# Optimization experiments

Measured on AMD Instinct MI355X. Metric: run time of the kernel, lower is better.

Reference implementation:

```python
import jax, jax.numpy as jnp
import numpy as np

NEG_SLOPE = 0.01  # torch nn.LeakyReLU default


def setup_inputs() -> dict:
    key = jax.random.key(0)
    kq, kk, kv, km, kw = jax.random.split(key, 5)
    B, Lq, Lk, Dk, Dv = 4, 2048, 2048, 512, 512
    q = jax.random.normal(kq, (B, Lq, Dk), dtype=jnp.float32)
    k = jax.random.normal(kk, (B, Lk, Dk), dtype=jnp.float32)
    v = jax.random.normal(kv, (B, Lk, Dv), dtype=jnp.float32)
    attn_mask = jax.random.randint(km, (B, Lq, Lk), 0, 2).astype(jnp.int32)
    # xavier_normal for (Dk, 1): std = sqrt(2 / (Dk + 1))
    weight = jax.random.normal(kw, (Dk, 1), dtype=jnp.float32) * np.sqrt(2.0 / (Dk + 1))
    return {"q": q, "k": k, "v": v, "attn_mask": attn_mask, "weight": weight}


def reference(q, k, v, attn_mask, weight):
    # (q - k) @ w  ==  (q @ w) - (k @ w): avoid the [B,Lq,Lk,Dk] intermediate.
    qw = jnp.einsum('bqd,do->bq', q, weight)  # [B, Lq]
    kw = jnp.einsum('bkd,do->bk', k, weight)  # [B, Lk]
    scores = qw[:, :, None] - kw[:, None, :]  # [B, Lq, Lk]
    attn = jnp.where(scores >= 0, scores, NEG_SLOPE * scores)  # LeakyReLU
    masked = attn_mask == 0
    attn = jnp.where(masked, -jnp.inf, attn)
    attn = jax.nn.softmax(attn, axis=2)
    attn = jnp.where(masked, 0.0, attn)
    # dropout omitted (eval mode / identity for reference correctness)
    output = jnp.einsum('bqk,bkd->bqd', attn, v)  # bmm
    return output, attn
```

## Files before the change

### kernel.cpp

```cpp
#include <hip/hip_runtime.h>
#include <math.h>

#define BB 4
#define LQ 2048
#define LK 2048
#define DK 512
#define DV 512

typedef __attribute__((ext_vector_type(8))) _Float16 f16x8;
typedef __attribute__((ext_vector_type(2))) _Float16 f16x2;
typedef __attribute__((ext_vector_type(4))) float f32x4;

#define WS_QW    0
#define WS_KW    8192
#define WS_M     16384
#define WS_INV   24576
#define WS_VF16  32768
#define WS_PART  2129920
#define NOUT     ((size_t)BB * LQ * DV)
#define WS_NEED(nks) (((size_t)WS_PART + (size_t)(nks) * NOUT) * 4)

__device__ __forceinline__ unsigned int pk2(float a, float b) {
    auto h = __builtin_amdgcn_cvt_pkrtz(a, b);
    return __builtin_bit_cast(unsigned int, h);
}

__global__ __launch_bounds__(256) void qkw_kernel(const float* __restrict__ q,
                                                  const float* __restrict__ k,
                                                  const float* __restrict__ w,
                                                  float* __restrict__ ws) {
    int gw   = (int)((blockIdx.x * blockDim.x + threadIdx.x) >> 6);
    int lane = threadIdx.x & 63;
    const int nq = BB * LQ;
    const float* row = (gw < nq) ? (q + (size_t)gw * DK) : (k + (size_t)(gw - nq) * DK);

    float acc = 0.f;
#pragma unroll
    for (int j = 0; j < DK; j += 256) {
        int idx = j + lane * 4;
        float4 rv = *reinterpret_cast<const float4*>(row + idx);
        float4 wv = *reinterpret_cast<const float4*>(w + idx);
        acc += rv.x * wv.x + rv.y * wv.y + rv.z * wv.z + rv.w * wv.w;
    }
#pragma unroll
    for (int off = 32; off >= 1; off >>= 1) acc += __shfl_xor(acc, off, 64);
    if (lane == 0) ws[gw] = acc;
}

__global__ __launch_bounds__(256) void vpack_kernel(const float* __restrict__ v,
                                                    unsigned short* __restrict__ vF) {
    __shared__ float tile[32][517];
    const int k32 = blockIdx.x;
    const int b   = blockIdx.y;
    const int k0  = k32 * 32;
    const int t   = threadIdx.x;

#pragma unroll
    for (int i = 0; i < 16; ++i) {
        int flat = i * 256 + t;
        int row  = flat >> 7;
        int c4   = flat & 127;
        float4 f = *reinterpret_cast<const float4*>(
            v + ((size_t)(b * LK + k0 + row)) * DV + c4 * 4);
        tile[row][c4 * 4 + 0] = f.x;
        tile[row][c4 * 4 + 1] = f.y;
        tile[row][c4 * 4 + 2] = f.z;
        tile[row][c4 * 4 + 3] = f.w;
    }
    __syncthreads();

    const int w = t >> 6, l = t & 63;
    const int rbase = (l >> 4) * 8;
#pragma unroll
    for (int f = 0; f < 8; ++f) {
        int n16 = w * 8 + f;
        int col = n16 * 16 + (l & 15);
        f16x8 vv;
#pragma unroll
        for (int j = 0; j < 8; ++j) vv[j] = (_Float16)tile[rbase + j][col];
        size_t u16base = (((size_t)(b * 32 + n16)) * 64 + k32) * 512;
        *reinterpret_cast<f16x8*>(vF + u16base + l * 8) = vv;
    }
}

__global__ __launch_bounds__(256) void rowstat_kernel(const int* __restrict__ mask,
                                                      float* __restrict__ ws,
                                                      float* __restrict__ attn) {
    __shared__ float kws[LK];
    const int b = (blockIdx.x * 4) / LQ;
    const int t = threadIdx.x;

    const float4* kw4 = reinterpret_cast<const float4*>(ws + WS_KW + b * LK);
#pragma unroll
    for (int i = 0; i < 2; ++i)
        reinterpret_cast<float4*>(kws)[t + i * 256] = kw4[t + i * 256];
    __syncthreads();

    const int wave = t >> 6, lane = t & 63;
    const int rid  = blockIdx.x * 4 + wave;
    const float qwv = ws[WS_QW + rid];
    const int* mrow = mask + (size_t)rid * LK;

    float m = -INFINITY, s = 0.f;
    unsigned int mybits = 0;
#pragma unroll
    for (int i = 0; i < 8; ++i) {
        int e = (i * 64 + lane) * 4;
        int4  mi = *reinterpret_cast<const int4*>(mrow + e);
        float4 kv = reinterpret_cast<const float4*>(kws)[i * 64 + lane];
        float vals[4] = {kv.x, kv.y, kv.z, kv.w};
        int   msks[4] = {mi.x, mi.y, mi.z, mi.w};

        unsigned int bits = (msks[0] ? 1u : 0u) | (msks[1] ? 2u : 0u) |
                            (msks[2] ? 4u : 0u) | (msks[3] ? 8u : 0u);
        mybits |= bits << (i * 4);

#pragma unroll
        for (int j = 0; j < 4; ++j) {
            float sc = qwv - vals[j];
            sc = fmaxf(sc, 0.01f * sc);
            if (msks[j]) {
                if (sc > m) { s = s * __expf(m - sc) + 1.f; m = sc; }
                else        { s += __expf(sc - m); }
            }
        }
    }
#pragma unroll
    for (int off = 32; off >= 1; off >>= 1) {
        float mo = __shfl_xor(m, off, 64);
        float so = __shfl_xor(s, off, 64);
        float M  = fmaxf(m, mo);
        float sa = (m  == M) ? s  : s  * __expf(m  - M);
        float sb = (mo == M) ? so : so * __expf(mo - M);
        m = M; s = sa + sb;
    }
    const float inv = (s > 0.f) ? 1.f / s : 0.f;
    if (lane == 0) {
        ws[WS_M   + rid] = m;
        ws[WS_INV + rid] = inv;
    }

    float* arow = attn + (size_t)rid * LK;
#pragma unroll
    for (int i = 0; i < 8; ++i) {
        float4 kv = reinterpret_cast<const float4*>(kws)[i * 64 + lane];
        float vals[4] = {kv.x, kv.y, kv.z, kv.w};
        unsigned int bits = (mybits >> (i * 4)) & 0xFu;
        float p[4];
#pragma unroll
        for (int j = 0; j < 4; ++j) {
            float sc = qwv - vals[j];
            sc = fmaxf(sc, 0.01f * sc);
            p[j] = (bits & (1u << j)) ? __expf(sc - m) * inv : 0.f;
        }
        *reinterpret_cast<float4*>(arow + (i * 64 + lane) * 4) =
            make_float4(p[0], p[1], p[2], p[3]);
    }
}

__global__ __launch_bounds__(512, 2) void pv_kernel(
        const float* __restrict__ attn,
        const unsigned short* __restrict__ vF,
        float* __restrict__ dst,
        int nks) {
    __shared__ unsigned int pH32[2][1024];
    __shared__ unsigned int pL32[2][1024];

    const int bid = blockIdx.x;
    const int ks  = bid & (nks - 1);
    const int rst = bid / nks;
    const int b   = rst & 3;
    const int qt  = rst >> 2;
    const int kspan  = LK / nks;
    const int ksteps = kspan >> 5;
    const int kbase  = ks * kspan;
    float* dstk = dst + (size_t)ks * NOUT;

    const int t = threadIdx.x;
    const int w = t >> 6, l = t & 63;

    const int m0   = t >> 8;
    const int lp   = (t >> 2) & 63;
    const int jp   = t & 3;
    const int row0 = m0 * 16 + (lp & 15);
    const int kk   = ((lp >> 4) << 3) + (jp << 1);
    const int rid0 = b * LQ + qt * 64 + row0;
    const int rid1 = rid0 + 32;

    const float* arow0 = attn + (size_t)rid0 * LK + kbase + kk;
    const float* arow1 = attn + (size_t)rid1 * LK + kbase + kk;

    const unsigned short* bsrc[4];
#pragma unroll
    for (int nb = 0; nb < 4; ++nb)
        bsrc[nb] = vF + (((size_t)(b * 32 + w * 4 + nb)) * 64 + (kbase >> 5)) * 512
                      + (size_t)l * 8;

    f16x8 bC[4], bN[4];
#pragma unroll
    for (int nb = 0; nb < 4; ++nb)
        bC[nb] = *reinterpret_cast<const f16x8*>(bsrc[nb]);

    {
        float2 a00 = *reinterpret_cast<const float2*>(arow0);
        float2 a01 = *reinterpret_cast<const float2*>(arow1);
        unsigned int h01 = pk2(a00.x, a00.y);
        f16x2 hv = __builtin_bit_cast(f16x2, h01);
        pH32[0][t] = h01;
        pL32[0][t] = pk2(a00.x - (float)hv[0], a00.y - (float)hv[1]);
        h01 = pk2(a01.x, a01.y);
        hv  = __builtin_bit_cast(f16x2, h01);
        pH32[0][t + 512] = h01;
        pL32[0][t + 512] = pk2(a01.x - (float)hv[0], a01.y - (float)hv[1]);
    }
    const int s1 = (ksteps > 1) ? 1 : 0;
    float2 aC0 = *reinterpret_cast<const float2*>(arow0 + s1 * 32);
    float2 aC1 = *reinterpret_cast<const float2*>(arow1 + s1 * 32);

    f32x4 acc[4][4];
#pragma unroll
    for (int mf = 0; mf < 4; ++mf)
#pragma unroll
        for (int nb = 0; nb < 4; ++nb)
            acc[mf][nb] = (f32x4){0.f, 0.f, 0.f, 0.f};

    __syncthreads();

    for (int s = 0; s < ksteps; ++s) {
        const int buf  = s & 1;
        const int nbuf = buf ^ 1;
        const int sn   = (s + 1 < ksteps) ? s + 1 : s;
        const int sn2  = (s + 2 < ksteps) ? s + 2 : s;

#pragma unroll
        for (int nb = 0; nb < 4; ++nb)
            bN[nb] = *reinterpret_cast<const f16x8*>(bsrc[nb] + (size_t)sn * 512);
        float2 aN0 = *reinterpret_cast<const float2*>(arow0 + sn2 * 32);
        float2 aN1 = *reinterpret_cast<const float2*>(arow1 + sn2 * 32);

        {
            unsigned int h01 = pk2(aC0.x, aC0.y);
            f16x2 hv = __builtin_bit_cast(f16x2, h01);
            pH32[nbuf][t] = h01;
            pL32[nbuf][t] = pk2(aC0.x - (float)hv[0], aC0.y - (float)hv[1]);
            h01 = pk2(aC1.x, aC1.y);
            hv  = __builtin_bit_cast(f16x2, h01);
            pH32[nbuf][t + 512] = h01;
            pL32[nbuf][t + 512] = pk2(aC1.x - (float)hv[0], aC1.y - (float)hv[1]);
        }

        const f16x8* pHf = reinterpret_cast<const f16x8*>(pH32[buf]);
        const f16x8* pLf = reinterpret_cast<const f16x8*>(pL32[buf]);
        f16x8 aH[4], aL[4];
#pragma unroll
        for (int mf = 0; mf < 4; ++mf) {
            aH[mf] = pHf[mf * 64 + l];
            aL[mf] = pLf[mf * 64 + l];
        }

        __builtin_amdgcn_s_setprio(1);
#pragma unroll
        for (int nb = 0; nb < 4; ++nb)
#pragma unroll
            for (int mf = 0; mf < 4; ++mf) {
                acc[mf][nb] = __builtin_amdgcn_mfma_f32_16x16x32_f16(aH[mf], bC[nb], acc[mf][nb], 0, 0, 0);
                acc[mf][nb] = __builtin_amdgcn_mfma_f32_16x16x32_f16(aL[mf], bC[nb], acc[mf][nb], 0, 0, 0);
            }
        __builtin_amdgcn_s_setprio(0);

        __syncthreads();

#pragma unroll
        for (int nb = 0; nb < 4; ++nb) bC[nb] = bN[nb];
        aC0 = aN0; aC1 = aN1;
    }

    float* obase = dstk + ((size_t)(b * LQ + qt * 64)) * DV + w * 64 + (l & 15);
#pragma unroll
    for (int mf = 0; mf < 4; ++mf)
#pragma unroll
        for (int nb = 0; nb < 4; ++nb)
#pragma unroll
            for (int r = 0; r < 4; ++r)
                obase[(size_t)(mf * 16 + (l >> 4) * 4 + r) * DV + nb * 16] = acc[mf][nb][r];
}

__global__ __launch_bounds__(256) void reduce_kernel(const float* __restrict__ parts,
                                                     float* __restrict__ out,
                                                     int nks) {
    const int n4 = (int)(NOUT / 4);
    int i = blockIdx.x * 256 + threadIdx.x;
    const float4* p = reinterpret_cast<const float4*>(parts);
    float4* o = reinterpret_cast<float4*>(out);
    for (; i < n4; i += 262144) {
        float4 s = p[i];
        for (int j = 1; j < nks; ++j) {
            float4 x = p[i + j * n4];
            s.x += x.x; s.y += x.y; s.z += x.z; s.w += x.w;
        }
        o[i] = s;
    }
}

extern "C" void kernel_launch(void* const* d_in, const int* in_sizes, int n_in,
                              void* d_out, int out_size, void* d_ws, size_t ws_size,
                              hipStream_t stream) {
    const float* q    = (const float*)d_in[0];
    const float* k    = (const float*)d_in[1];
    const float* v    = (const float*)d_in[2];
    const int*   mask = (const int*)d_in[3];
    const float* w    = (const float*)d_in[4];

    float* out  = (float*)d_out;
    float* attn = out + NOUT;
    float* ws   = (float*)d_ws;

    unsigned short* vF = (unsigned short*)(ws + WS_VF16);
    float* part = ws + WS_PART;

    qkw_kernel<<<4096, 256, 0, stream>>>(q, k, w, ws);
    vpack_kernel<<<dim3(64, 4), 256, 0, stream>>>(v, vF);
    rowstat_kernel<<<2048, 256, 0, stream>>>(mask, ws, attn);

    if (ws_size >= WS_NEED(4)) {
        pv_kernel<<<512, 512, 0, stream>>>(attn, vF, part, 4);
        reduce_kernel<<<1024, 256, 0, stream>>>(part, out, 4);
    } else if (ws_size >= WS_NEED(2)) {
        pv_kernel<<<256, 512, 0, stream>>>(attn, vF, part, 2);
        reduce_kernel<<<1024, 256, 0, stream>>>(part, out, 2);
    } else {
        pv_kernel<<<128, 512, 0, stream>>>(attn, vF, out, 1);
    }
}
```

Measured before the change: 93.29 us.

## Replace split-K PV with output-column split and drop reduction kernel

The PV matmul no longer splits the key dimension into partial sums that a separate reduce kernel adds up. Each block now covers the full K range for a 64-row by 128-column output tile, using 256 threads with wider float4 attention loads. This removes the partial-buffer writes, the reduction pass and one launch. The cost is that every block re-reads the full attention rows, so attention traffic is four times higher, and the dependency chain per block is longer.

```diff
diff --git a/kernel.cpp b/kernel.cpp
--- a/kernel.cpp
+++ b/kernel.cpp
@@ -16,9 +16,7 @@
 #define WS_M     16384
 #define WS_INV   24576
 #define WS_VF16  32768
-#define WS_PART  2129920
 #define NOUT     ((size_t)BB * LQ * DV)
-#define WS_NEED(nks) (((size_t)WS_PART + (size_t)(nks) * NOUT) * 4)
 
 __device__ __forceinline__ unsigned int pk2(float a, float b) {
     auto h = __builtin_amdgcn_cvt_pkrtz(a, b);
@@ -158,70 +156,65 @@
     }
 }
 
-__global__ __launch_bounds__(512, 2) void pv_kernel(
+__global__ __launch_bounds__(256, 2) void pv_kernel(
         const float* __restrict__ attn,
         const unsigned short* __restrict__ vF,
-        float* __restrict__ dst,
-        int nks) {
+        float* __restrict__ out) {
     __shared__ unsigned int pH32[2][1024];
     __shared__ unsigned int pL32[2][1024];
 
     const int bid = blockIdx.x;
-    const int ks  = bid & (nks - 1);
-    const int rst = bid / nks;
-    const int b   = rst & 3;
-    const int qt  = rst >> 2;
-    const int kspan  = LK / nks;
-    const int ksteps = kspan >> 5;
-    const int kbase  = ks * kspan;
-    float* dstk = dst + (size_t)ks * NOUT;
+    const int ns  = bid & 3;
+    const int b   = (bid >> 2) & 3;
+    const int qt  = bid >> 4;
+    const int ksteps = LK >> 5;
 
     const int t = threadIdx.x;
     const int w = t >> 6, l = t & 63;
 
-    const int m0   = t >> 8;
-    const int lp   = (t >> 2) & 63;
-    const int jp   = t & 3;
-    const int row0 = m0 * 16 + (lp & 15);
-    const int kk   = ((lp >> 4) << 3) + (jp << 1);
-    const int rid0 = b * LQ + qt * 64 + row0;
-    const int rid1 = rid0 + 32;
-
-    const float* arow0 = attn + (size_t)rid0 * LK + kbase + kk;
-    const float* arow1 = attn + (size_t)rid1 * LK + kbase + kk;
-
-    const unsigned short* bsrc[4];
-#pragma unroll
-    for (int nb = 0; nb < 4; ++nb)
-        bsrc[nb] = vF + (((size_t)(b * 32 + w * 4 + nb)) * 64 + (kbase >> 5)) * 512
+    const int row_a = (t >> 6) * 16 + (t & 15);
+    const int kb    = ((t >> 4) & 3) * 8;
+    const int rid   = b * LQ + qt * 64 + row_a;
+    const float* arow = attn + (size_t)rid * LK + kb;
+
+    const unsigned short* bsrc[2];
+#pragma unroll
+    for (int nb = 0; nb < 2; ++nb)
+        bsrc[nb] = vF + (((size_t)(b * 32 + ns * 8 + w * 2 + nb)) * 64) * 512
                       + (size_t)l * 8;
 
-    f16x8 bC[4], bN[4];
-#pragma unroll
-    for (int nb = 0; nb < 4; ++nb)
+    auto stage = [&](const float4& x, const float4& y, int buf) {
+        unsigned int H[4], L[4];
+        float f[8] = {x.x, x.y, x.z, x.w, y.x, y.y, y.z, y.w};
+#pragma unroll
+        for (int jw = 0; jw < 4; ++jw) {
+            unsigned int h01 = pk2(f[2 * jw], f[2 * jw + 1]);
+            f16x2 hv = __builtin_bit_cast(f16x2, h01);
+            H[jw] = h01;
+            L[jw] = pk2(f[2 * jw] - (float)hv[0], f[2 * jw + 1] - (float)hv[1]);
+        }
+        *reinterpret_cast<uint4*>(&pH32[buf][t * 4]) = *reinterpret_cast<uint4*>(H);
+        *reinterpret_cast<uint4*>(&pL32[buf][t * 4]) = *reinterpret_cast<uint4*>(L);
+    };
+
+    f16x8 bC[2], bN[2];
+#pragma unroll
+    for (int nb = 0; nb < 2; ++nb)
         bC[nb] = *reinterpret_cast<const f16x8*>(bsrc[nb]);
 
     {
-        float2 a00 = *reinterpret_cast<const float2*>(arow0);
-        float2 a01 = *reinterpret_cast<const float2*>(arow1);
-        unsigned int h01 = pk2(a00.x, a00.y);
-        f16x2 hv = __builtin_bit_cast(f16x2, h01);
-        pH32[0][t] = h01;
-        pL32[0][t] = pk2(a00.x - (float)hv[0], a00.y - (float)hv[1]);
-        h01 = pk2(a01.x, a01.y);
-        hv  = __builtin_bit_cast(f16x2, h01);
-        pH32[0][t + 512] = h01;
-        pL32[0][t + 512] = pk2(a01.x - (float)hv[0], a01.y - (float)hv[1]);
-    }
-    const int s1 = (ksteps > 1) ? 1 : 0;
-    float2 aC0 = *reinterpret_cast<const float2*>(arow0 + s1 * 32);
-    float2 aC1 = *reinterpret_cast<const float2*>(arow1 + s1 * 32);
-
-    f32x4 acc[4][4];
+        float4 x = *reinterpret_cast<const float4*>(arow);
+        float4 y = *reinterpret_cast<const float4*>(arow + 4);
+        stage(x, y, 0);
+    }
+    float4 aCx = *reinterpret_cast<const float4*>(arow + 32);
+    float4 aCy = *reinterpret_cast<const float4*>(arow + 36);
+
+    f32x4 acc[4][2];
 #pragma unroll
     for (int mf = 0; mf < 4; ++mf)
 #pragma unroll
-        for (int nb = 0; nb < 4; ++nb)
+        for (int nb = 0; nb < 2; ++nb)
             acc[mf][nb] = (f32x4){0.f, 0.f, 0.f, 0.f};
 
     __syncthreads();
@@ -233,21 +226,12 @@
         const int sn2  = (s + 2 < ksteps) ? s + 2 : s;
 
 #pragma unroll
-        for (int nb = 0; nb < 4; ++nb)
+        for (int nb = 0; nb < 2; ++nb)
             bN[nb] = *reinterpret_cast<const f16x8*>(bsrc[nb] + (size_t)sn * 512);
-        float2 aN0 = *reinterpret_cast<const float2*>(arow0 + sn2 * 32);
-        float2 aN1 = *reinterpret_cast<const float2*>(arow1 + sn2 * 32);
-
-        {
-            unsigned int h01 = pk2(aC0.x, aC0.y);
-            f16x2 hv = __builtin_bit_cast(f16x2, h01);
-            pH32[nbuf][t] = h01;
-            pL32[nbuf][t] = pk2(aC0.x - (float)hv[0], aC0.y - (float)hv[1]);
-            h01 = pk2(aC1.x, aC1.y);
-            hv  = __builtin_bit_cast(f16x2, h01);
-            pH32[nbuf][t + 512] = h01;
-            pL32[nbuf][t + 512] = pk2(aC1.x - (float)hv[0], aC1.y - (float)hv[1]);
-        }
+        float4 aNx = *reinterpret_cast<const float4*>(arow + sn2 * 32);
+        float4 aNy = *reinterpret_cast<const float4*>(arow + sn2 * 32 + 4);
+
+        stage(aCx, aCy, nbuf);
 
         const f16x8* pHf = reinterpret_cast<const f16x8*>(pH32[buf]);
         const f16x8* pLf = reinterpret_cast<const f16x8*>(pL32[buf]);
@@ -260,7 +244,7 @@
 
         __builtin_amdgcn_s_setprio(1);
 #pragma unroll
-        for (int nb = 0; nb < 4; ++nb)
+        for (int nb = 0; nb < 2; ++nb)
 #pragma unroll
             for (int mf = 0; mf < 4; ++mf) {
                 acc[mf][nb] = __builtin_amdgcn_mfma_f32_16x16x32_f16(aH[mf], bC[nb], acc[mf][nb], 0, 0, 0);
@@ -271,35 +255,19 @@
         __syncthreads();
 
 #pragma unroll
-        for (int nb = 0; nb < 4; ++nb) bC[nb] = bN[nb];
-        aC0 = aN0; aC1 = aN1;
-    }
-
-    float* obase = dstk + ((size_t)(b * LQ + qt * 64)) * DV + w * 64 + (l & 15);
+        for (int nb = 0; nb < 2; ++nb) bC[nb] = bN[nb];
+        aCx = aNx; aCy = aNy;
+    }
+
+    float* obase = out + ((size_t)(b * LQ + qt * 64)) * DV
+                       + ns * 128 + w * 32 + (l & 15);
 #pragma unroll
     for (int mf = 0; mf < 4; ++mf)
 #pragma unroll
-        for (int nb = 0; nb < 4; ++nb)
+        for (int nb = 0; nb < 2; ++nb)
 #pragma unroll
             for (int r = 0; r < 4; ++r)
                 obase[(size_t)(mf * 16 + (l >> 4) * 4 + r) * DV + nb * 16] = acc[mf][nb][r];
-}
-
-__global__ __launch_bounds__(256) void reduce_kernel(const float* __restrict__ parts,
-                                                     float* __restrict__ out,
-                                                     int nks) {
-    const int n4 = (int)(NOUT / 4);
-    int i = blockIdx.x * 256 + threadIdx.x;
-    const float4* p = reinterpret_cast<const float4*>(parts);
-    float4* o = reinterpret_cast<float4*>(out);
-    for (; i < n4; i += 262144) {
-        float4 s = p[i];
-        for (int j = 1; j < nks; ++j) {
-            float4 x = p[i + j * n4];
-            s.x += x.x; s.y += x.y; s.z += x.z; s.w += x.w;
-        }
-        o[i] = s;
-    }
 }
 
 extern "C" void kernel_launch(void* const* d_in, const int* in_sizes, int n_in,
@@ -316,19 +284,9 @@
     float* ws   = (float*)d_ws;
 
     unsigned short* vF = (unsigned short*)(ws + WS_VF16);
-    float* part = ws + WS_PART;
 
     qkw_kernel<<<4096, 256, 0, stream>>>(q, k, w, ws);
     vpack_kernel<<<dim3(64, 4), 256, 0, stream>>>(v, vF);
     rowstat_kernel<<<2048, 256, 0, stream>>>(mask, ws, attn);
-
-    if (ws_size >= WS_NEED(4)) {
-        pv_kernel<<<512, 512, 0, stream>>>(attn, vF, part, 4);
-        reduce_kernel<<<1024, 256, 0, stream>>>(part, out, 4);
-    } else if (ws_size >= WS_NEED(2)) {
-        pv_kernel<<<256, 512, 0, stream>>>(attn, vF, part, 2);
-        reduce_kernel<<<1024, 256, 0, stream>>>(part, out, 2);
-    } else {
-        pv_kernel<<<128, 512, 0, stream>>>(attn, vF, out, 1);
-    }
-}
+    pv_kernel<<<512, 256, 0, stream>>>(attn, vF, out);
+}
```

Measured after the change: 84.22 us. -9.7%, faster.
